# Kernel tuning notes

Hardware: AMD Instinct MI355X
Metric: run time of the kernel (lower is better)

The kernel has to match this reference:

```python
import jax, jax.numpy as jnp
import numpy as np

N_HEAD = 16
HEAD_DIM = 64  # n_embd // n_head = 1024 // 16


def setup_inputs() -> dict:
    key = jax.random.key(0)
    k1, k2, k3 = jax.random.split(key, 3)
    B, S, D = 2, 2048, 1024
    x = jax.random.normal(k1, (B, S, D), dtype=jnp.float32)
    # torch nn.Linear stores weight [out, in]; we keep [in, out] for x @ W
    w_qkv = jax.random.normal(k2, (D, 3 * D), dtype=jnp.float32) * (D ** -0.5)
    w_proj = jax.random.normal(k3, (D, D), dtype=jnp.float32) * (D ** -0.5)
    return {"x": x, "w_qkv": w_qkv, "w_proj": w_proj}


def reference(x, w_qkv, w_proj):
    B, S, D = x.shape
    qkv = x @ w_qkv  # [B, S, 3D]
    q, k, v = jnp.split(qkv, 3, axis=-1)
    # [B, H, S, hd]
    q = q.reshape(B, S, N_HEAD, HEAD_DIM).transpose(0, 2, 1, 3)
    k = k.reshape(B, S, N_HEAD, HEAD_DIM).transpose(0, 2, 1, 3)
    v = v.reshape(B, S, N_HEAD, HEAD_DIM).transpose(0, 2, 1, 3)
    att = jnp.einsum('bhid,bhjd->bhij', q, k) * (HEAD_DIM ** -0.5)
    causal = jnp.tril(jnp.ones((S, S), dtype=bool))
    att = jnp.where(causal, att, jnp.finfo(att.dtype).min)
    att = jax.nn.softmax(att, axis=-1)
    # dropout p=0 (eval) -> identity
    y = jnp.einsum('bhij,bhjd->bhid', att, v)
    y = y.transpose(0, 2, 1, 3).reshape(B, S, D)
    return y @ w_proj
```

## Files before the change

kernel.cpp:

```cpp
#include <hip/hip_runtime.h>

#define AS1 __attribute__((address_space(1)))
#define AS3 __attribute__((address_space(3)))

using f32x4 = __attribute__((ext_vector_type(4))) float;
using s16x8 = __attribute__((ext_vector_type(8))) short;
using u16x4 = __attribute__((ext_vector_type(4))) unsigned short;
using u32x2 = __attribute__((ext_vector_type(2))) unsigned int;

__device__ __forceinline__ unsigned short f2bf(float f) {
  union { float f; unsigned u; } v; v.f = f;
  unsigned u = v.u;
  return (unsigned short)((u + 0x7FFFu + ((u >> 16) & 1u)) >> 16);
}

__device__ __forceinline__ unsigned pack_bf2(float a, float b) {
  union { float f; unsigned u; } x, y; x.f = a; y.f = b;
  return (x.u >> 16) | (y.u & 0xFFFF0000u);
}

__device__ __forceinline__ void load_lds16(const void* g, void* l) {
  __builtin_amdgcn_global_load_lds((const AS1 void*)g, (AS3 void*)l, 16, 0, 0);
}

__global__ __launch_bounds__(256) void prep_kernel(const float* __restrict__ x,
                                                   const float* __restrict__ w_qkv,
                                                   const float* __restrict__ w_proj,
                                                   unsigned short* __restrict__ xb,
                                                   unsigned short* __restrict__ wqkvT,
                                                   unsigned short* __restrict__ wprojT) {
  __shared__ float tile[32][33];
  const int bid = blockIdx.x, tid = threadIdx.x;
  if (bid < 4096) {
    int i = bid * 256 + tid;
    float4 v = ((const float4*)x)[i];
    u16x4 o;
    o.x = f2bf(v.x); o.y = f2bf(v.y); o.z = f2bf(v.z); o.w = f2bf(v.w);
    ((u16x4*)xb)[i] = o;
    return;
  }
  const float* in;
  unsigned short* out;
  int bx, by, R, C;
  if (bid < 7168) {
    int t = bid - 4096;
    bx = t % 96; by = t / 96; R = 1024; C = 3072;
    in = w_qkv; out = wqkvT;
  } else {
    int t = bid - 7168;
    bx = t % 32; by = t / 32; R = 1024; C = 1024;
    in = w_proj; out = wprojT;
  }
  const int tx = tid & 31, ty = tid >> 5;
  int xcol = bx * 32 + tx;
  int y0 = by * 32;
  for (int j = ty; j < 32; j += 8)
    tile[j][tx] = in[(size_t)(y0 + j) * C + xcol];
  __syncthreads();
  int x2 = by * 32 + tx;
  int y2 = bx * 32;
  for (int j = ty; j < 32; j += 8)
    out[(size_t)(y2 + j) * R + x2] = f2bf(tile[tx][j]);
}

__global__ __launch_bounds__(256) void transpose_v(const unsigned short* __restrict__ qkv,
                                                   unsigned short* __restrict__ Vt) {
  __shared__ unsigned short tile[64][65];
  const int tid = threadIdx.x;
  const int bh = blockIdx.y, b = bh >> 4, h = bh & 15;
  const int s0 = blockIdx.x * 64;
#pragma unroll
  for (int it = 0; it < 2; ++it) {
    int c = tid + it * 256;
    int row = c >> 3, cc = c & 7;
    s16x8 v = *(const s16x8*)(qkv + (size_t)(b * 2048 + s0 + row) * 3072 + 2048 + h * 64 + cc * 8);
#pragma unroll
    for (int j = 0; j < 8; ++j) tile[row][cc * 8 + j] = (unsigned short)v[j];
  }
  __syncthreads();
#pragma unroll
  for (int it = 0; it < 2; ++it) {
    int c = tid + it * 256;
    int d = c >> 3, sc = c & 7;
    s16x8 o;
#pragma unroll
    for (int j = 0; j < 8; ++j) o[j] = (short)tile[sc * 8 + j][d];
    *(s16x8*)(Vt + (size_t)bh * 64 * 2048 + (size_t)d * 2048 + s0 + sc * 8) = o;
  }
}

__global__ __launch_bounds__(256) void gemm_qkv(const unsigned short* __restrict__ A,
                                                const unsigned short* __restrict__ Bt,
                                                unsigned short* __restrict__ C,
                                                int M, int N, int K) {
  __shared__ unsigned short As[128 * 64];
  __shared__ unsigned short Bs[128 * 64];
  const int tid = threadIdx.x;
  const int wave = tid >> 6, lane = tid & 63;
  const int l15 = lane & 15, quad = lane >> 4;
  const int sx = l15 & 7;
  const int wm = wave & 1, wn = wave >> 1;
  const int bm = blockIdx.y, bn = blockIdx.x;

  f32x4 acc[4][4] = {};

  for (int k0 = 0; k0 < K; k0 += 64) {
    __syncthreads();
#pragma unroll
    for (int s = 0; s < 4; ++s) {
      int c = tid + s * 256;
      int row = c >> 3, cc = c & 7;
      int kc = (cc ^ (row & 7)) * 8;
      load_lds16(A + (size_t)(bm * 128 + row) * K + k0 + kc, As + c * 8);
      load_lds16(Bt + (size_t)(bn * 128 + row) * K + k0 + kc, Bs + c * 8);
    }
    __syncthreads();
#pragma unroll
    for (int kk = 0; kk < 2; ++kk) {
      s16x8 af[4], bfr[4];
#pragma unroll
      for (int i = 0; i < 4; ++i) {
        af[i]  = *(const s16x8*)(As + (wm * 64 + i * 16 + l15) * 64 + ((quad + 4 * kk) ^ sx) * 8);
        bfr[i] = *(const s16x8*)(Bs + (wn * 64 + i * 16 + l15) * 64 + ((quad + 4 * kk) ^ sx) * 8);
      }
#pragma unroll
      for (int i = 0; i < 4; ++i)
#pragma unroll
        for (int j = 0; j < 4; ++j)
          acc[i][j] = __builtin_amdgcn_mfma_f32_16x16x32_bf16(af[i], bfr[j], acc[i][j], 0, 0, 0);
    }
  }

  const int row0 = bm * 128 + wm * 64 + quad * 4;
  const int col0 = bn * 128 + wn * 64 + l15;
#pragma unroll
  for (int i = 0; i < 4; ++i)
#pragma unroll
    for (int j = 0; j < 4; ++j)
#pragma unroll
      for (int r = 0; r < 4; ++r)
        C[(size_t)(row0 + i * 16 + r) * N + (col0 + j * 16)] = f2bf(acc[i][j][r]);
}

__global__ __launch_bounds__(256) void gemm_proj(const unsigned short* __restrict__ A,
                                                 const unsigned short* __restrict__ Bt,
                                                 float* __restrict__ C,
                                                 int M, int N, int K) {
  __shared__ unsigned short As[128 * 64];
  __shared__ unsigned short Bs[64 * 64];
  const int tid = threadIdx.x;
  const int wave = tid >> 6, lane = tid & 63;
  const int l15 = lane & 15, quad = lane >> 4;
  const int sx = l15 & 7;
  const int wm = wave & 1, wn = wave >> 1;
  const int bm = blockIdx.y, bn = blockIdx.x;

  f32x4 acc[4][2] = {};

  for (int k0 = 0; k0 < K; k0 += 64) {
    __syncthreads();
#pragma unroll
    for (int s = 0; s < 4; ++s) {
      int c = tid + s * 256;
      int row = c >> 3, cc = c & 7;
      int kc = (cc ^ (row & 7)) * 8;
      load_lds16(A + (size_t)(bm * 128 + row) * K + k0 + kc, As + c * 8);
    }
#pragma unroll
    for (int s = 0; s < 2; ++s) {
      int c = tid + s * 256;
      int row = c >> 3, cc = c & 7;
      int kc = (cc ^ (row & 7)) * 8;
      load_lds16(Bt + (size_t)(bn * 64 + row) * K + k0 + kc, Bs + c * 8);
    }
    __syncthreads();
#pragma unroll
    for (int kk = 0; kk < 2; ++kk) {
      s16x8 af[4], bfr[2];
#pragma unroll
      for (int i = 0; i < 4; ++i)
        af[i] = *(const s16x8*)(As + (wm * 64 + i * 16 + l15) * 64 + ((quad + 4 * kk) ^ sx) * 8);
#pragma unroll
      for (int j = 0; j < 2; ++j)
        bfr[j] = *(const s16x8*)(Bs + (wn * 32 + j * 16 + l15) * 64 + ((quad + 4 * kk) ^ sx) * 8);
#pragma unroll
      for (int i = 0; i < 4; ++i)
#pragma unroll
        for (int j = 0; j < 2; ++j)
          acc[i][j] = __builtin_amdgcn_mfma_f32_16x16x32_bf16(af[i], bfr[j], acc[i][j], 0, 0, 0);
    }
  }

  const int row0 = bm * 128 + wm * 64 + quad * 4;
  const int col0 = bn * 64 + wn * 32 + l15;
#pragma unroll
  for (int i = 0; i < 4; ++i)
#pragma unroll
    for (int j = 0; j < 2; ++j)
#pragma unroll
      for (int r = 0; r < 4; ++r)
        C[(size_t)(row0 + i * 16 + r) * N + (col0 + j * 16)] = acc[i][j][r];
}

__global__ __launch_bounds__(256) void attn_kernel(const unsigned short* __restrict__ qkv,
                                                   const unsigned short* __restrict__ Vt,
                                                   unsigned short* __restrict__ Y) {
  __shared__ unsigned short Qs[64 * 64];
  __shared__ unsigned short Ks[2][64 * 64];
  __shared__ unsigned short Vs[2][64 * 64];
  const int tid = threadIdx.x;
  const int wave = tid >> 6, lane = tid & 63;
  const int l15 = lane & 15, quad = lane >> 4;
  const int sx = l15 & 7, sx2 = sx << 1;

  const int p = blockIdx.x;
  const int bh = p & 31;
  const int u = (p >> 5) & 7;
  const int hi = p >> 8;
  const int lq = (hi == 0) ? u : (hi == 1) ? (15 - u) : (hi == 2) ? (16 + u) : (31 - u);
  const int q0 = lq * 64;
  const int b = bh >> 4, h = bh & 15;
  const size_t base = (size_t)b * 2048 * 3072 + h * 64;
  const size_t vbase = (size_t)bh * 64 * 2048;

#pragma unroll
  for (int s = 0; s < 2; ++s) {
    int c = tid + s * 256;
    int row = c >> 3, cc = c & 7;
    int kc = (cc ^ (row & 7)) * 8;
    load_lds16(qkv + base + (size_t)(q0 + row) * 3072 + kc, Qs + c * 8);
    load_lds16(qkv + base + (size_t)row * 3072 + 1024 + kc, Ks[0] + c * 8);
    load_lds16(Vt + vbase + (size_t)row * 2048 + kc, Vs[0] + c * 8);
  }
  __syncthreads();

  s16x8 qf[2];
  qf[0] = *(const s16x8*)(Qs + (wave * 16 + l15) * 64 + ((quad    ) ^ sx) * 8);
  qf[1] = *(const s16x8*)(Qs + (wave * 16 + l15) * 64 + ((quad + 4) ^ sx) * 8);

  f32x4 o[4] = {};
  float m_i = -1e30f, l_i = 0.f;
  const float kScale = 0.125f * 1.44269504f;
  const int qrow_w0 = q0 + wave * 16;
  const int qrow = qrow_w0 + l15;
  unsigned short* Pw = Qs + wave * 16 * 64;

  int cur = 0;
  for (int j0 = 0; j0 <= q0; j0 += 64) {
    if (j0 < q0) {
#pragma unroll
      for (int s = 0; s < 2; ++s) {
        int c = tid + s * 256;
        int row = c >> 3, cc = c & 7;
        int kc = (cc ^ (row & 7)) * 8;
        load_lds16(qkv + base + (size_t)(j0 + 64 + row) * 3072 + 1024 + kc, Ks[cur ^ 1] + c * 8);
        load_lds16(Vt + vbase + (size_t)row * 2048 + (j0 + 64) + kc, Vs[cur ^ 1] + c * 8);
      }
    }

    const unsigned short* Kc = Ks[cur];
    const unsigned short* Vc = Vs[cur];
    f32x4 s[4];
#pragma unroll
    for (int nt = 0; nt < 4; ++nt) {
      const int kr = nt * 16 + l15;
      s16x8 kf0 = *(const s16x8*)(Kc + kr * 64 + ((quad    ) ^ sx) * 8);
      s16x8 kf1 = *(const s16x8*)(Kc + kr * 64 + ((quad + 4) ^ sx) * 8);
      f32x4 z = {};
      z = __builtin_amdgcn_mfma_f32_16x16x32_bf16(kf0, qf[0], z, 0, 0, 0);
      z = __builtin_amdgcn_mfma_f32_16x16x32_bf16(kf1, qf[1], z, 0, 0, 0);
      s[nt] = z;
    }

    if (j0 + 63 > qrow_w0) {
#pragma unroll
      for (int nt = 0; nt < 4; ++nt) {
        int key0 = j0 + nt * 16 + quad * 4;
#pragma unroll
        for (int r = 0; r < 4; ++r)
          if (key0 + r > qrow) s[nt][r] = -3e38f;
      }
    }

    float t0 = fmaxf(fmaxf(s[0][0], s[0][1]), fmaxf(s[0][2], s[0][3]));
    float t1 = fmaxf(fmaxf(s[1][0], s[1][1]), fmaxf(s[1][2], s[1][3]));
    float t2 = fmaxf(fmaxf(s[2][0], s[2][1]), fmaxf(s[2][2], s[2][3]));
    float t3 = fmaxf(fmaxf(s[3][0], s[3][1]), fmaxf(s[3][2], s[3][3]));
    float tmax = fmaxf(fmaxf(t0, t1), fmaxf(t2, t3));
    tmax = fmaxf(tmax, __shfl_xor(tmax, 16, 64));
    tmax = fmaxf(tmax, __shfl_xor(tmax, 32, 64));

    if (!__all(tmax <= m_i)) {
      float mn = fmaxf(m_i, tmax);
      float alpha = __builtin_amdgcn_exp2f((m_i - mn) * kScale);
      m_i = mn;
      l_i *= alpha;
#pragma unroll
      for (int dt = 0; dt < 4; ++dt)
#pragma unroll
        for (int r = 0; r < 4; ++r)
          o[dt][r] *= alpha;
    }
    const float mk = m_i * kScale;
    float rs[4] = {0.f, 0.f, 0.f, 0.f};
#pragma unroll
    for (int nt = 0; nt < 4; ++nt)
#pragma unroll
      for (int r = 0; r < 4; ++r) {
        float pv = __builtin_amdgcn_exp2f(__builtin_fmaf(s[nt][r], kScale, -mk));
        s[nt][r] = pv;
        rs[nt] += pv;
      }
    float rsum = (rs[0] + rs[1]) + (rs[2] + rs[3]);
    rsum += __shfl_xor(rsum, 16, 64);
    rsum += __shfl_xor(rsum, 32, 64);
    l_i += rsum;

#pragma unroll
    for (int nt = 0; nt < 4; ++nt) {
      u32x2 pk;
      pk.x = pack_bf2(s[nt][0], s[nt][1]);
      pk.y = pack_bf2(s[nt][2], s[nt][3]);
      int phys = (nt * 4 + quad) ^ sx2;
      *(u32x2*)(Pw + l15 * 64 + phys * 4) = pk;
    }

    s16x8 pf[2];
    pf[0] = *(const s16x8*)(Pw + l15 * 64 + (((quad * 2)    ) ^ sx2) * 4);
    pf[1] = *(const s16x8*)(Pw + l15 * 64 + (((quad * 2) + 8) ^ sx2) * 4);

#pragma unroll
    for (int dt = 0; dt < 4; ++dt) {
      const int vr = dt * 16 + l15;
      s16x8 vf0 = *(const s16x8*)(Vc + vr * 64 + ((quad    ) ^ sx) * 8);
      s16x8 vf1 = *(const s16x8*)(Vc + vr * 64 + ((quad + 4) ^ sx) * 8);
      o[dt] = __builtin_amdgcn_mfma_f32_16x16x32_bf16(vf0, pf[0], o[dt], 0, 0, 0);
      o[dt] = __builtin_amdgcn_mfma_f32_16x16x32_bf16(vf1, pf[1], o[dt], 0, 0, 0);
    }

    __syncthreads();
    cur ^= 1;
  }

  const float inv = 1.0f / l_i;
  const size_t yoff = (size_t)(b * 2048 + qrow) * 1024 + h * 64 + quad * 4;
#pragma unroll
  for (int dt = 0; dt < 4; ++dt) {
    u16x4 pk;
#pragma unroll
    for (int r = 0; r < 4; ++r) pk[r] = f2bf(o[dt][r] * inv);
    *(u16x4*)(Y + yoff + dt * 16) = pk;
  }
}

extern "C" void kernel_launch(void* const* d_in, const int* in_sizes, int n_in,
                              void* d_out, int out_size, void* d_ws, size_t ws_size,
                              hipStream_t stream) {
  const float* x      = (const float*)d_in[0];
  const float* w_qkv  = (const float*)d_in[1];
  const float* w_proj = (const float*)d_in[2];
  char* ws = (char*)d_ws;
  unsigned short* xb     = (unsigned short*)(ws);
  unsigned short* wqkvT  = (unsigned short*)(ws + (size_t)(8  << 20));
  unsigned short* wprojT = (unsigned short*)(ws + (size_t)(14 << 20));
  unsigned short* qkv    = (unsigned short*)(ws + (size_t)(16 << 20));
  unsigned short* y      = (unsigned short*)(ws + (size_t)(40 << 20));
  unsigned short* Vt     = (unsigned short*)(ws + (size_t)(48 << 20));

  prep_kernel<<<8192, 256, 0, stream>>>(x, w_qkv, w_proj, xb, wqkvT, wprojT);
  gemm_qkv<<<dim3(24, 32), 256, 0, stream>>>(xb, wqkvT, qkv, 4096, 3072, 1024);
  transpose_v<<<dim3(32, 32), 256, 0, stream>>>(qkv, Vt);
  attn_kernel<<<1024, 256, 0, stream>>>(qkv, Vt, y);
  gemm_proj<<<dim3(16, 32), 256, 0, stream>>>(y, wprojT, (float*)d_out, 4096, 1024, 1024);
}
```

Measured before the change: 191.1 us.

## Triple-buffer K/V tiles in attention with vmcnt waits and a single barrier

Switches the attention kernel's K/V shared-memory staging from double to triple buffering, so tiles are prefetched two iterations ahead. Manual s_waitcnt vmcnt plus one s_barrier at the top of each iteration replace the trailing __syncthreads. Q fragments are now loaded straight from global memory into registers instead of going through LDS, and P gets its own scratch buffer. The aim is to hide global load latency and cut synchronization. The cost is more LDS per block, which may lower occupancy, and correctness now depends on the vmcnt counting matching the four loads issued per stage.

```diff
diff --git a/kernel.cpp b/kernel.cpp
--- a/kernel.cpp
+++ b/kernel.cpp
@@ -205,9 +205,9 @@
 __global__ __launch_bounds__(256) void attn_kernel(const unsigned short* __restrict__ qkv,
                                                    const unsigned short* __restrict__ Vt,
                                                    unsigned short* __restrict__ Y) {
-  __shared__ unsigned short Qs[64 * 64];
-  __shared__ unsigned short Ks[2][64 * 64];
-  __shared__ unsigned short Vs[2][64 * 64];
+  __shared__ unsigned short Ps[4 * 16 * 64];
+  __shared__ unsigned short Ks[3][64 * 64];
+  __shared__ unsigned short Vs[3][64 * 64];
   const int tid = threadIdx.x;
   const int wave = tid >> 6, lane = tid & 63;
   const int l15 = lane & 15, quad = lane >> 4;
@@ -222,44 +222,56 @@
   const int b = bh >> 4, h = bh & 15;
   const size_t base = (size_t)b * 2048 * 3072 + h * 64;
   const size_t vbase = (size_t)bh * 64 * 2048;
-
-#pragma unroll
-  for (int s = 0; s < 2; ++s) {
-    int c = tid + s * 256;
-    int row = c >> 3, cc = c & 7;
-    int kc = (cc ^ (row & 7)) * 8;
-    load_lds16(qkv + base + (size_t)(q0 + row) * 3072 + kc, Qs + c * 8);
-    load_lds16(qkv + base + (size_t)row * 3072 + 1024 + kc, Ks[0] + c * 8);
-    load_lds16(Vt + vbase + (size_t)row * 2048 + kc, Vs[0] + c * 8);
-  }
-  __syncthreads();
-
+  const int nt_tiles = lq + 1;
+
+  const int c0 = tid, c1 = tid + 256;
+  const int row0_ = c0 >> 3, cc0_ = c0 & 7, kc0 = (cc0_ ^ (row0_ & 7)) * 8;
+  const int row1_ = c1 >> 3, cc1_ = c1 & 7, kc1 = (cc1_ ^ (row1_ & 7)) * 8;
+
+  const unsigned short* qptr = qkv + base + (size_t)(q0 + wave * 16 + l15) * 3072 + quad * 8;
   s16x8 qf[2];
-  qf[0] = *(const s16x8*)(Qs + (wave * 16 + l15) * 64 + ((quad    ) ^ sx) * 8);
-  qf[1] = *(const s16x8*)(Qs + (wave * 16 + l15) * 64 + ((quad + 4) ^ sx) * 8);
+  qf[0] = *(const s16x8*)(qptr);
+  qf[1] = *(const s16x8*)(qptr + 32);
+
+  {
+    load_lds16(qkv + base + (size_t)(0 + row0_) * 3072 + 1024 + kc0, Ks[0] + c0 * 8);
+    load_lds16(Vt + vbase + (size_t)row0_ * 2048 + 0 + kc0, Vs[0] + c0 * 8);
+    load_lds16(qkv + base + (size_t)(0 + row1_) * 3072 + 1024 + kc1, Ks[0] + c1 * 8);
+    load_lds16(Vt + vbase + (size_t)row1_ * 2048 + 0 + kc1, Vs[0] + c1 * 8);
+    if (nt_tiles > 1) {
+      load_lds16(qkv + base + (size_t)(64 + row0_) * 3072 + 1024 + kc0, Ks[1] + c0 * 8);
+      load_lds16(Vt + vbase + (size_t)row0_ * 2048 + 64 + kc0, Vs[1] + c0 * 8);
+      load_lds16(qkv + base + (size_t)(64 + row1_) * 3072 + 1024 + kc1, Ks[1] + c1 * 8);
+      load_lds16(Vt + vbase + (size_t)row1_ * 2048 + 64 + kc1, Vs[1] + c1 * 8);
+    }
+  }
 
   f32x4 o[4] = {};
   float m_i = -1e30f, l_i = 0.f;
   const float kScale = 0.125f * 1.44269504f;
   const int qrow_w0 = q0 + wave * 16;
   const int qrow = qrow_w0 + l15;
-  unsigned short* Pw = Qs + wave * 16 * 64;
-
-  int cur = 0;
-  for (int j0 = 0; j0 <= q0; j0 += 64) {
-    if (j0 < q0) {
-#pragma unroll
-      for (int s = 0; s < 2; ++s) {
-        int c = tid + s * 256;
-        int row = c >> 3, cc = c & 7;
-        int kc = (cc ^ (row & 7)) * 8;
-        load_lds16(qkv + base + (size_t)(j0 + 64 + row) * 3072 + 1024 + kc, Ks[cur ^ 1] + c * 8);
-        load_lds16(Vt + vbase + (size_t)row * 2048 + (j0 + 64) + kc, Vs[cur ^ 1] + c * 8);
-      }
-    }
-
-    const unsigned short* Kc = Ks[cur];
-    const unsigned short* Vc = Vs[cur];
+  unsigned short* Pw = Ps + wave * 16 * 64;
+
+  int slot = 0;
+  int slot2 = 2;
+  for (int t = 0; t < nt_tiles; ++t) {
+    const int j0 = t * 64;
+    if (t + 1 < nt_tiles) asm volatile("s_waitcnt vmcnt(4)" ::: "memory");
+    else                  asm volatile("s_waitcnt vmcnt(0)" ::: "memory");
+    __builtin_amdgcn_s_barrier();
+    __builtin_amdgcn_sched_barrier(0);
+
+    if (t + 2 < nt_tiles) {
+      const int j2 = j0 + 128;
+      load_lds16(qkv + base + (size_t)(j2 + row0_) * 3072 + 1024 + kc0, Ks[slot2] + c0 * 8);
+      load_lds16(Vt + vbase + (size_t)row0_ * 2048 + j2 + kc0, Vs[slot2] + c0 * 8);
+      load_lds16(qkv + base + (size_t)(j2 + row1_) * 3072 + 1024 + kc1, Ks[slot2] + c1 * 8);
+      load_lds16(Vt + vbase + (size_t)row1_ * 2048 + j2 + kc1, Vs[slot2] + c1 * 8);
+    }
+
+    const unsigned short* Kc = Ks[slot];
+    const unsigned short* Vc = Vs[slot];
     f32x4 s[4];
 #pragma unroll
     for (int nt = 0; nt < 4; ++nt) {
@@ -338,8 +350,8 @@
       o[dt] = __builtin_amdgcn_mfma_f32_16x16x32_bf16(vf1, pf[1], o[dt], 0, 0, 0);
     }
 
-    __syncthreads();
-    cur ^= 1;
+    slot = (slot == 2) ? 0 : slot + 1;
+    slot2 = (slot2 == 2) ? 0 : slot2 + 1;
   }
 
   const float inv = 1.0f / l_i;
```

Result: no change. 192.4 us (+0.6%).
